# Performance work log

Measured on AMD Instinct MI355X. Metric: run time of the kernel, lower is better.

## Reference

```python
import jax, jax.numpy as jnp
import numpy as np
import math

NUM_HEADS = 8
WINDOW_SIZE = 1025
GLOBAL_TOKENS = 512  # effectively min(4, GLOBAL_TOKENS) indices are used, as in the torch code


def setup_inputs() -> dict:
    key = jax.random.key(0)
    k0, k1, k2 = jax.random.split(key, 3)
    B, C, H, W = 2, 256, 64, 64
    x = jax.random.normal(k0, (B, C, H, W), dtype=jnp.float32)
    # proj1: Linear(C, 3C); proj2: Linear(C, C). Stored as [in, out] matrices.
    w1 = jax.random.normal(k1, (C, 3 * C), dtype=jnp.float32) * 0.02
    b1 = jnp.zeros((3 * C,), dtype=jnp.float32)
    w2 = jax.random.normal(k2, (C, C), dtype=jnp.float32) * 0.02
    b2 = jnp.zeros((C,), dtype=jnp.float32)
    return {"x": x, "w1": w1, "b1": b1, "w2": w2, "b2": b2}


def _longformer_bias(L, W, window_size, global_tokens, dtype):
    # band: |i - j| <= window_size // 2  (matches start/end loop in torch code)
    i = jnp.arange(L)
    band = jnp.abs(i[:, None] - i[None, :]) <= (window_size // 2)
    gidx = [0, W - 1, L - W, L - 1][:global_tokens]
    g = jnp.zeros((L,), dtype=bool).at[jnp.array(gidx)].set(True)
    mask = band | g[:, None] | g[None, :]
    return jnp.where(mask, jnp.array(0.0, dtype), jnp.array(-jnp.inf, dtype))


def reference(x, w1, b1, w2, b2):
    B, C, H, W = x.shape
    L = H * W
    hd = C // NUM_HEADS
    # b c h w -> b (h w) c
    xt = x.reshape(B, C, L).transpose(0, 2, 1)
    qkv = xt @ w1 + b1  # [B, L, 3C]
    # 'b L (C H K)' with K=3, H=heads: last dim factors as (head_dim, heads, 3)
    qkv = qkv.reshape(B, L, hd, NUM_HEADS, 3).transpose(4, 0, 3, 1, 2)  # [3, B, Hh, L, hd]
    q, k, v = qkv[0], qkv[1], qkv[2]
    bias = _longformer_bias(L, W, WINDOW_SIZE, GLOBAL_TOKENS, x.dtype)
    scale = math.sqrt(hd)
    attn = jnp.einsum('bhqc,bhkc->bhqk', q, k) / scale + bias
    attn = jax.nn.softmax(attn, axis=-1)
    o = jnp.einsum('bhqk,bhkc->bhqc', attn, v)  # [B, Hh, L, hd]
    # 'b H (h w) C -> b h w (C H)': channel index = c*num_heads + head
    o = o.transpose(0, 2, 3, 1).reshape(B, H, W, hd * NUM_HEADS)
    out = o @ w2 + b2  # [B, H, W, C]
    return out.transpose(0, 3, 1, 2)  # b h w C -> b C h w
```

## Files before the change

### kernel.cpp

```cpp
#include <hip/hip_runtime.h>
#include <hip/hip_bf16.h>

#define BB 2
#define CC 256
#define HEADS 8
#define HD 32
#define LL 4096
#define HALF_WIN 512

using short8  = __attribute__((ext_vector_type(8))) short;
using float4v = __attribute__((ext_vector_type(4))) float;

__device__ __forceinline__ ushort f2bf(float x) {
    uint u = __float_as_uint(x);
    u += 0x7fff + ((u >> 16) & 1);
    return (ushort)(u >> 16);
}
__device__ __forceinline__ float ubf(ushort u) {
    return __uint_as_float((uint)u << 16);
}

__global__ __launch_bounds__(256) void wt_kernel(const float* __restrict__ w1,
                                                 const float* __restrict__ w2,
                                                 ushort* __restrict__ w1t,
                                                 ushort* __restrict__ w2t) {
    __shared__ float tl[16][17];
    const int tx = threadIdx.x & 15, ty = threadIdx.x >> 4;
    const int ci0 = blockIdx.x * 16;
    const int y = blockIdx.y;
    if (y < 48) {
        int j0 = y * 16;
        tl[ty][tx] = w1[(size_t)(ci0 + ty) * 768 + j0 + tx];
        __syncthreads();
        w1t[(size_t)(j0 + ty) * CC + ci0 + tx] = f2bf(tl[tx][ty]);
    } else {
        int co0 = (y - 48) * 16;
        tl[ty][tx] = w2[(size_t)(ci0 + ty) * CC + co0 + tx];
        __syncthreads();
        w2t[(size_t)(co0 + ty) * CC + ci0 + tx] = f2bf(tl[tx][ty]);
    }
}

__global__ __launch_bounds__(256) void qkv_kernel(const float* __restrict__ x,
                                                  const ushort* __restrict__ w1t,
                                                  const float* __restrict__ b1,
                                                  ushort* __restrict__ qb,
                                                  ushort* __restrict__ kb,
                                                  ushort* __restrict__ vt) {
    __shared__ __align__(16) ushort xs[64 * 264];
    const int dg = blockIdx.x;
    const int l0 = blockIdx.y * 64;
    const int b  = blockIdx.z;
    const int t  = threadIdx.x;
    const int w  = t >> 6, ln = t & 63, c = ln & 15, g = ln >> 4;

    {
        const int l  = t & 63;
        const int cg = (t >> 6) * 4;
#pragma unroll
        for (int p = 0; p < 16; p++) {
            int c0 = p * 16 + cg;
            ushort4 v4;
            v4.x = f2bf(x[((size_t)b * CC + c0 + 0) * LL + l0 + l]);
            v4.y = f2bf(x[((size_t)b * CC + c0 + 1) * LL + l0 + l]);
            v4.z = f2bf(x[((size_t)b * CC + c0 + 2) * LL + l0 + l]);
            v4.w = f2bf(x[((size_t)b * CC + c0 + 3) * LL + l0 + l]);
            *(ushort4*)&xs[l * 264 + c0] = v4;
        }
    }
    __syncthreads();

    const int jbase = dg * 192 + w * 48;
    float4v acc[3][4] = {};
#pragma unroll
    for (int ks = 0; ks < 8; ks++) {
        short8 af[3], bfr[4];
#pragma unroll
        for (int jt = 0; jt < 3; jt++)
            af[jt] = *(const short8*)(w1t + (size_t)(jbase + jt * 16 + c) * CC + ks * 32 + g * 8);
#pragma unroll
        for (int lt = 0; lt < 4; lt++)
            bfr[lt] = *(const short8*)&xs[(lt * 16 + c) * 264 + ks * 32 + g * 8];
#pragma unroll
        for (int jt = 0; jt < 3; jt++)
#pragma unroll
            for (int lt = 0; lt < 4; lt++)
                acc[jt][lt] = __builtin_amdgcn_mfma_f32_16x16x32_bf16(af[jt], bfr[lt], acc[jt][lt], 0, 0, 0);
    }
    __syncthreads();

    ushort* qs  = xs;
    ushort* ksm = xs + 64 * 72;
    ushort* vs  = xs + 2 * 64 * 72;

#pragma unroll
    for (int jt = 0; jt < 3; jt++) {
#pragma unroll
        for (int r = 0; r < 4; r++) {
            int j = jbase + jt * 16 + g * 4 + r;
            float bias = b1[j];
            int t3 = j % 3, h = (j / 3) & 7, dl = (j / 24) & 7;
            int slot = h * 8 + dl;
#pragma unroll
            for (int lt = 0; lt < 4; lt++) {
                int l = lt * 16 + c;
                ushort u = f2bf(acc[jt][lt][r] + bias);
                if (t3 == 0)      qs[l * 72 + slot]  = u;
                else if (t3 == 1) ksm[l * 72 + slot] = u;
                else              vs[l * 74 + slot]  = u;
            }
        }
    }
    __syncthreads();

    {
        const int l = t & 63;
#pragma unroll
        for (int p = 0; p < 2; p++) {
            int h = p * 4 + (t >> 6);
            size_t rowq = (((size_t)(b * 8 + h) * 4 + dg) * LL + l0 + l) * 8;
            *(short8*)(qb + rowq) = *(const short8*)&qs[l * 72 + h * 8];
            *(short8*)(kb + rowq) = *(const short8*)&ksm[l * 72 + h * 8];
        }
#pragma unroll
        for (int p = 0; p < 16; p++) {
            int hd = p * 4 + (t >> 6);
            vt[((size_t)(b * 8 + (hd >> 3)) * HD + dg * 8 + (hd & 7)) * LL + l0 + l] = vs[l * 74 + hd];
        }
    }
}

__global__ __launch_bounds__(256) void attn_kernel(const ushort* __restrict__ qb,
                                                   const ushort* __restrict__ kb,
                                                   const ushort* __restrict__ vt,
                                                   ushort* __restrict__ obuf) {
    __shared__ __align__(16) ushort pshare[4][640];
    const int it = blockIdx.x;
    const int bh = blockIdx.y;
    const int i0 = it * 64;
    const int t  = threadIdx.x;
    const int w  = t >> 6;
    const int ln = t & 63;
    const int c  = ln & 15;
    const int g  = ln >> 4;

    const size_t slab = ((size_t)bh * 4 + g) * LL;
    const int i = i0 + w * 16 + c;
    const bool iglob = (i == 0) | (i == 63) | (i == LL - 64) | (i == LL - 1);

    const short8 qf = *(const short8*)(qb + (slab + i) * 8);

    float4v o0 = {0.f, 0.f, 0.f, 0.f}, o1 = {0.f, 0.f, 0.f, 0.f};
    float dsum = 0.f;

    int t0, t1, ne = 0;
    int extra[4];
    t0 = it * 4 - 32; if (t0 < 0) t0 = 0;
    t1 = it * 4 + 35; if (t1 > 255) t1 = 255;
    const int gt[4] = {0, 3, 252, 255};
#pragma unroll
    for (int e = 0; e < 4; e++)
        if (gt[e] < t0 || gt[e] > t1) extra[ne++] = gt[e];
    const int nbt = t1 - t0 + 1;
    const int nt = nbt + ne;
    const int npair = (nt + 1) >> 1;

    ushort* wb = &pshare[w][0];
    const float scale = 0.17677669529663687f;
    const ushort* vb = vt + (size_t)bh * HD * LL;

    for (int m = 0; m < npair; m++) {
        const int n0 = 2 * m, n1 = 2 * m + 1;
        const int tA = (n0 < nbt) ? t0 + n0 : extra[n0 - nbt];
        const bool vBv = (n1 < nt);
        const int tB = (n1 < nbt) ? t0 + n1 : (vBv ? extra[n1 - nbt] : t0);

        const short8 kfA = *(const short8*)(kb + (slab + tA * 16 + c) * 8);
        const short8 kfB = *(const short8*)(kb + (slab + tB * 16 + c) * 8);
        float4v zero = {0.f, 0.f, 0.f, 0.f};
        float4v sA = __builtin_amdgcn_mfma_f32_16x16x32_bf16(kfA, qf, zero, 0, 0, 0);
        float4v sB = __builtin_amdgcn_mfma_f32_16x16x32_bf16(kfB, qf, zero, 0, 0, 0);

        float pA[4], pB[4];
#pragma unroll
        for (int r = 0; r < 4; r++) {
            int j = tA * 16 + g * 4 + r;
            bool band = (unsigned)(i - j + HALF_WIN) <= 2u * HALF_WIN;
            bool jg = (j == 0) | (j == 63) | (j == LL - 64) | (j == LL - 1);
            pA[r] = (band | jg | iglob) ? __expf(sA[r] * scale) : 0.f;
            dsum += pA[r];
        }
#pragma unroll
        for (int r = 0; r < 4; r++) {
            int j = tB * 16 + g * 4 + r;
            bool band = (unsigned)(i - j + HALF_WIN) <= 2u * HALF_WIN;
            bool jg = (j == 0) | (j == 63) | (j == LL - 64) | (j == LL - 1);
            pB[r] = (vBv & (band | jg | iglob)) ? __expf(sB[r] * scale) : 0.f;
            dsum += pB[r];
        }

        uint2 ua, ub2;
        ua.x  = (uint)f2bf(pA[0]) | ((uint)f2bf(pA[1]) << 16);
        ua.y  = (uint)f2bf(pA[2]) | ((uint)f2bf(pA[3]) << 16);
        ub2.x = (uint)f2bf(pB[0]) | ((uint)f2bf(pB[1]) << 16);
        ub2.y = (uint)f2bf(pB[2]) | ((uint)f2bf(pB[3]) << 16);
        *(uint2*)&wb[c * 40 + 4 * g]      = ua;
        *(uint2*)&wb[c * 40 + 16 + 4 * g] = ub2;

        const short8 pf = *(const short8*)&wb[c * 40 + 8 * g];

        const int jv = (g < 2) ? tA * 16 + g * 8 : tB * 16 + (g - 2) * 8;
        const short8 v0f = *(const short8*)(vb + (size_t)c * LL + jv);
        const short8 v1f = *(const short8*)(vb + (size_t)(16 + c) * LL + jv);
        o0 = __builtin_amdgcn_mfma_f32_16x16x32_bf16(pf, v0f, o0, 0, 0, 0);
        o1 = __builtin_amdgcn_mfma_f32_16x16x32_bf16(pf, v1f, o1, 0, 0, 0);
    }

    dsum += __shfl_xor(dsum, 16);
    dsum += __shfl_xor(dsum, 32);

    const int b = bh >> 3, hh = bh & 7;
#pragma unroll
    for (int r = 0; r < 4; r++) {
        float dn = __shfl(dsum, g * 4 + r);
        float inv = 1.0f / dn;
        int irow = i0 + w * 16 + g * 4 + r;
        size_t rowb = ((size_t)b * LL + irow) * CC;
        obuf[rowb + (size_t)c * 8 + hh]        = f2bf(o0[r] * inv);
        obuf[rowb + (size_t)(16 + c) * 8 + hh] = f2bf(o1[r] * inv);
    }
}

__global__ __launch_bounds__(256) void attn_global_partial(const ushort* __restrict__ qb,
                                                           const ushort* __restrict__ kb,
                                                           const ushort* __restrict__ vt,
                                                           float* __restrict__ gpart) {
    __shared__ float qs[4][32];
    __shared__ float sc[4][256];
    const int ch = blockIdx.x;
    const int bh = blockIdx.y;
    const int t  = threadIdx.x;
    const int gidx[4] = {0, 63, LL - 64, LL - 1};
    const float scale = 0.17677669529663687f;

    if (t < 128) {
        int r = t >> 5, dd = t & 31;
        int i = gidx[r];
        qs[r][dd] = ubf(qb[(((size_t)bh * 4 + (dd >> 3)) * LL + i) * 8 + (dd & 7)]);
    }
    __syncthreads();

    const int j = ch * 256 + t;
    float dot[4] = {};
#pragma unroll
    for (int s = 0; s < 4; s++) {
        const short8 kf = *(const short8*)(kb + (((size_t)bh * 4 + s) * LL + j) * 8);
#pragma unroll
        for (int e = 0; e < 8; e++) {
            float kv = ubf((ushort)kf[e]);
#pragma unroll
            for (int r = 0; r < 4; r++) dot[r] += qs[r][s * 8 + e] * kv;
        }
    }
#pragma unroll
    for (int r = 0; r < 4; r++) sc[r][t] = __expf(dot[r] * scale);
    __syncthreads();

    const int w = t >> 6, ln = t & 63;
    float den = sc[w][ln] + sc[w][ln + 64] + sc[w][ln + 128] + sc[w][ln + 192];
#pragma unroll
    for (int o = 1; o < 64; o <<= 1) den += __shfl_xor(den, o);

    const int dd = ln & 31, half = ln >> 5;
    float acc = 0.f;
    const ushort* vrow = vt + ((size_t)bh * HD + dd) * LL + ch * 256 + half * 128;
#pragma unroll
    for (int q8 = 0; q8 < 16; q8++) {
        const short8 v8 = *(const short8*)(vrow + q8 * 8);
#pragma unroll
        for (int e = 0; e < 8; e++) acc += sc[w][half * 128 + q8 * 8 + e] * ubf((ushort)v8[e]);
    }
    acc += __shfl_xor(acc, 32);

    float* gp = gpart + (((size_t)bh * 16 + ch) * 4 + w) * 33;
    if (ln < 32) gp[dd] = acc;
    if (ln == 0) gp[32] = den;
}

__global__ __launch_bounds__(128) void attn_global_combine(const float* __restrict__ gpart,
                                                           ushort* __restrict__ obuf) {
    const int bh = blockIdx.x;
    const int t  = threadIdx.x;
    const int r  = t >> 5, dd = t & 31;
    const int gidx[4] = {0, 63, LL - 64, LL - 1};
    float pv = 0.f, den = 0.f;
#pragma unroll
    for (int ch = 0; ch < 16; ch++) {
        const float* gp = gpart + (((size_t)bh * 16 + ch) * 4 + r) * 33;
        pv  += gp[dd];
        den += gp[32];
    }
    const int b = bh >> 3, hh = bh & 7, i = gidx[r];
    obuf[((size_t)b * LL + i) * CC + dd * 8 + hh] = f2bf(pv / den);
}

__global__ __launch_bounds__(256) void proj_kernel(const ushort* __restrict__ obuf,
                                                   const ushort* __restrict__ w2t,
                                                   const float* __restrict__ b2,
                                                   float* __restrict__ out) {
    const int co0 = blockIdx.x * 16;
    const int l0  = blockIdx.y * 256 + (threadIdx.x >> 6) * 64;
    const int b   = blockIdx.z;
    const int ln  = threadIdx.x & 63;
    const int c   = ln & 15, g = ln >> 4;

    float4v acc[4] = {};
    const ushort* arow = w2t + (size_t)(co0 + c) * CC + g * 8;
    const ushort* brow = obuf + ((size_t)b * LL + l0 + c) * CC + g * 8;
#pragma unroll
    for (int ks = 0; ks < 8; ks++) {
        const short8 af = *(const short8*)(arow + ks * 32);
#pragma unroll
        for (int nf = 0; nf < 4; nf++) {
            const short8 bf = *(const short8*)(brow + (size_t)nf * 16 * CC + ks * 32);
            acc[nf] = __builtin_amdgcn_mfma_f32_16x16x32_bf16(af, bf, acc[nf], 0, 0, 0);
        }
    }
#pragma unroll
    for (int nf = 0; nf < 4; nf++) {
#pragma unroll
        for (int r = 0; r < 4; r++) {
            int co = co0 + g * 4 + r;
            int l  = l0 + nf * 16 + c;
            out[((size_t)b * CC + co) * LL + l] = acc[nf][r] + b2[co];
        }
    }
}

extern "C" void kernel_launch(void* const* d_in, const int* in_sizes, int n_in,
                              void* d_out, int out_size, void* d_ws, size_t ws_size,
                              hipStream_t stream) {
    const float* x  = (const float*)d_in[0];
    const float* w1 = (const float*)d_in[1];
    const float* b1 = (const float*)d_in[2];
    const float* w2 = (const float*)d_in[3];
    const float* b2 = (const float*)d_in[4];
    float* out = (float*)d_out;

    const size_t QKE = (size_t)BB * HEADS * LL * HD;
    const size_t OBE = (size_t)BB * LL * CC;
    ushort* qb  = (ushort*)d_ws;
    ushort* kb  = qb + QKE;
    ushort* vt  = kb + QKE;
    ushort* ob  = vt + QKE;
    float*  gp  = (float*)(ob + OBE);
    ushort* w2t = (ushort*)(gp + 16 * 16 * 4 * 33);
    ushort* w1t = w2t + CC * CC;

    wt_kernel<<<dim3(16, 64), 256, 0, stream>>>(w1, w2, w1t, w2t);
    qkv_kernel<<<dim3(4, 64, 2), 256, 0, stream>>>(x, w1t, b1, qb, kb, vt);
    attn_kernel<<<dim3(64, 16), 256, 0, stream>>>(qb, kb, vt, ob);
    attn_global_partial<<<dim3(16, 16), 256, 0, stream>>>(qb, kb, vt, gp);
    attn_global_combine<<<dim3(16), 128, 0, stream>>>(gp, ob);
    proj_kernel<<<dim3(16, 16, 2), 256, 0, stream>>>(ob, w2t, b2, out);
}
```

Before: 148.5 us.

## Split attention into unmasked interior tiles, fold softmax scale into Q

```diff
diff --git a/kernel.cpp b/kernel.cpp
--- a/kernel.cpp
+++ b/kernel.cpp
@@ -19,6 +19,8 @@
 __device__ __forceinline__ float ubf(ushort u) {
     return __uint_as_float((uint)u << 16);
 }
+
+#define QSCALE 0.25503485f
 
 __global__ __launch_bounds__(256) void wt_kernel(const float* __restrict__ w1,
                                                  const float* __restrict__ w2,
@@ -104,7 +106,9 @@
 #pragma unroll
             for (int lt = 0; lt < 4; lt++) {
                 int l = lt * 16 + c;
-                ushort u = f2bf(acc[jt][lt][r] + bias);
+                float val = acc[jt][lt][r] + bias;
+                if (t3 == 0) val *= QSCALE;
+                ushort u = f2bf(val);
                 if (t3 == 0)      qs[l * 72 + slot]  = u;
                 else if (t3 == 1) ksm[l * 72 + slot] = u;
                 else              vs[l * 74 + slot]  = u;
@@ -135,8 +139,9 @@
                                                    const ushort* __restrict__ vt,
                                                    ushort* __restrict__ obuf) {
     __shared__ __align__(16) ushort pshare[4][640];
-    const int it = blockIdx.x;
-    const int bh = blockIdx.y;
+    const int n  = blockIdx.x;
+    const int bh = ((n & 7) << 1) | ((n >> 3) & 1);
+    const int it = n >> 4;
     const int i0 = it * 64;
     const int t  = threadIdx.x;
     const int w  = t >> 6;
@@ -146,37 +151,67 @@
 
     const size_t slab = ((size_t)bh * 4 + g) * LL;
     const int i = i0 + w * 16 + c;
-    const bool iglob = (i == 0) | (i == 63) | (i == LL - 64) | (i == LL - 1);
 
     const short8 qf = *(const short8*)(qb + (slab + i) * 8);
 
     float4v o0 = {0.f, 0.f, 0.f, 0.f}, o1 = {0.f, 0.f, 0.f, 0.f};
     float dsum = 0.f;
 
-    int t0, t1, ne = 0;
-    int extra[4];
-    t0 = it * 4 - 32; if (t0 < 0) t0 = 0;
-    t1 = it * 4 + 35; if (t1 > 255) t1 = 255;
+    int t0 = it * 4 - 32; if (t0 < 0) t0 = 0;
+    int t1 = it * 4 + 35; if (t1 > 255) t1 = 255;
+    int tf0 = it * 4 - 28; if (tf0 < 0) tf0 = 0;
+    int tf1 = it * 4 + 31; if (tf1 > 255) tf1 = 255;
+
+    int ml[12], nm = 0;
+    for (int tt = t0; tt < tf0; tt++) ml[nm++] = tt;
+    for (int tt = tf1 + 1; tt <= t1; tt++) ml[nm++] = tt;
     const int gt[4] = {0, 3, 252, 255};
 #pragma unroll
     for (int e = 0; e < 4; e++)
-        if (gt[e] < t0 || gt[e] > t1) extra[ne++] = gt[e];
-    const int nbt = t1 - t0 + 1;
-    const int nt = nbt + ne;
-    const int npair = (nt + 1) >> 1;
+        if (gt[e] < t0 || gt[e] > t1) ml[nm++] = gt[e];
 
     ushort* wb = &pshare[w][0];
-    const float scale = 0.17677669529663687f;
     const ushort* vb = vt + (size_t)bh * HD * LL;
 
-    for (int m = 0; m < npair; m++) {
-        const int n0 = 2 * m, n1 = 2 * m + 1;
-        const int tA = (n0 < nbt) ? t0 + n0 : extra[n0 - nbt];
-        const bool vBv = (n1 < nt);
-        const int tB = (n1 < nbt) ? t0 + n1 : (vBv ? extra[n1 - nbt] : t0);
-
-        const short8 kfA = *(const short8*)(kb + (slab + tA * 16 + c) * 8);
-        const short8 kfB = *(const short8*)(kb + (slab + tB * 16 + c) * 8);
+    const int npair_f = (tf1 - tf0 + 1) >> 1;
+    const ushort* kp  = kb + (slab + (size_t)(tf0 * 16 + c)) * 8;
+    const ushort* vp0 = vb + (size_t)c * LL + tf0 * 16 + g * 8;
+    const ushort* vp1 = vp0 + 16 * LL;
+    for (int m = 0; m < npair_f; m++) {
+        const short8 kfA = *(const short8*)kp;
+        const short8 kfB = *(const short8*)(kp + 128);
+        kp += 256;
+        float4v zero = {0.f, 0.f, 0.f, 0.f};
+        float4v sA = __builtin_amdgcn_mfma_f32_16x16x32_bf16(kfA, qf, zero, 0, 0, 0);
+        float4v sB = __builtin_amdgcn_mfma_f32_16x16x32_bf16(kfB, qf, zero, 0, 0, 0);
+
+        float pA[4], pB[4];
+#pragma unroll
+        for (int r = 0; r < 4; r++) { pA[r] = exp2f(sA[r]); dsum += pA[r]; }
+#pragma unroll
+        for (int r = 0; r < 4; r++) { pB[r] = exp2f(sB[r]); dsum += pB[r]; }
+
+        uint2 ua, ub2;
+        ua.x  = (uint)f2bf(pA[0]) | ((uint)f2bf(pA[1]) << 16);
+        ua.y  = (uint)f2bf(pA[2]) | ((uint)f2bf(pA[3]) << 16);
+        ub2.x = (uint)f2bf(pB[0]) | ((uint)f2bf(pB[1]) << 16);
+        ub2.y = (uint)f2bf(pB[2]) | ((uint)f2bf(pB[3]) << 16);
+        *(uint2*)&wb[c * 40 + 4 * g]      = ua;
+        *(uint2*)&wb[c * 40 + 16 + 4 * g] = ub2;
+
+        const short8 pf = *(const short8*)&wb[c * 40 + 8 * g];
+
+        const short8 v0f = *(const short8*)vp0;
+        const short8 v1f = *(const short8*)vp1;
+        vp0 += 32; vp1 += 32;
+        o0 = __builtin_amdgcn_mfma_f32_16x16x32_bf16(pf, v0f, o0, 0, 0, 0);
+        o1 = __builtin_amdgcn_mfma_f32_16x16x32_bf16(pf, v1f, o1, 0, 0, 0);
+    }
+
+    for (int m = 0; m < nm; m += 2) {
+        const int tA = ml[m], tB = ml[m + 1];
+        const short8 kfA = *(const short8*)(kb + (slab + (size_t)(tA * 16 + c)) * 8);
+        const short8 kfB = *(const short8*)(kb + (slab + (size_t)(tB * 16 + c)) * 8);
         float4v zero = {0.f, 0.f, 0.f, 0.f};
         float4v sA = __builtin_amdgcn_mfma_f32_16x16x32_bf16(kfA, qf, zero, 0, 0, 0);
         float4v sB = __builtin_amdgcn_mfma_f32_16x16x32_bf16(kfB, qf, zero, 0, 0, 0);
@@ -187,7 +222,7 @@
             int j = tA * 16 + g * 4 + r;
             bool band = (unsigned)(i - j + HALF_WIN) <= 2u * HALF_WIN;
             bool jg = (j == 0) | (j == 63) | (j == LL - 64) | (j == LL - 1);
-            pA[r] = (band | jg | iglob) ? __expf(sA[r] * scale) : 0.f;
+            pA[r] = (band | jg) ? exp2f(sA[r]) : 0.f;
             dsum += pA[r];
         }
 #pragma unroll
@@ -195,7 +230,7 @@
             int j = tB * 16 + g * 4 + r;
             bool band = (unsigned)(i - j + HALF_WIN) <= 2u * HALF_WIN;
             bool jg = (j == 0) | (j == 63) | (j == LL - 64) | (j == LL - 1);
-            pB[r] = (vBv & (band | jg | iglob)) ? __expf(sB[r] * scale) : 0.f;
+            pB[r] = (band | jg) ? exp2f(sB[r]) : 0.f;
             dsum += pB[r];
         }
 
@@ -241,7 +276,6 @@
     const int bh = blockIdx.y;
     const int t  = threadIdx.x;
     const int gidx[4] = {0, 63, LL - 64, LL - 1};
-    const float scale = 0.17677669529663687f;
 
     if (t < 128) {
         int r = t >> 5, dd = t & 31;
@@ -263,7 +297,7 @@
         }
     }
 #pragma unroll
-    for (int r = 0; r < 4; r++) sc[r][t] = __expf(dot[r] * scale);
+    for (int r = 0; r < 4; r++) sc[r][t] = exp2f(dot[r]);
     __syncthreads();
 
     const int w = t >> 6, ln = t & 63;
@@ -359,7 +393,7 @@
 
     wt_kernel<<<dim3(16, 64), 256, 0, stream>>>(w1, w2, w1t, w2t);
     qkv_kernel<<<dim3(4, 64, 2), 256, 0, stream>>>(x, w1t, b1, qb, kb, vt);
-    attn_kernel<<<dim3(64, 16), 256, 0, stream>>>(qb, kb, vt, ob);
+    attn_kernel<<<dim3(1024), 256, 0, stream>>>(qb, kb, vt, ob);
     attn_global_partial<<<dim3(16, 16), 256, 0, stream>>>(qb, kb, vt, gp);
     attn_global_combine<<<dim3(16), 128, 0, stream>>>(gp, ob);
     proj_kernel<<<dim3(16, 16, 2), 256, 0, stream>>>(ob, w2t, b2, out);
```

New measurement: 145.1 us. 2.3% less time.
